# Performance work log

Measured on AMD Instinct MI355X. Metric: run time of the kernel, lower is better.

Reference implementation:

```python
import jax, jax.numpy as jnp
import numpy as np

IN_FEATURES = 4096
OUT_FEATURES = 1024
BATCH = 16384
WERR = 1.0
BERR = 1.0


def setup_inputs() -> dict:
    key = jax.random.key(0)
    kx, kw = jax.random.split(key)
    X = jax.random.normal(kx, (BATCH, IN_FEATURES), dtype=jnp.float32)
    # glorot_uniform init for W, zeros for bias (as in Keras layer)
    limit = np.sqrt(6.0 / (IN_FEATURES + OUT_FEATURES)).astype(np.float32)
    W = jax.random.uniform(kw, (IN_FEATURES, OUT_FEATURES), dtype=jnp.float32,
                           minval=-limit, maxval=limit)
    bias = jnp.zeros((1, OUT_FEATURES), dtype=jnp.float32)
    return {"X": X, "W": W, "bias": bias}


def reference(X, W, bias):
    # Binarize weights/bias with sign(), scaled by Werr/Berr, then dense matmul.
    Wb = jnp.sign(W) * WERR          # [in, out], values in {-1, 0, +1}
    bb = jnp.sign(bias) * BERR       # [1, out]
    Z = jnp.matmul(X, Wb) + bb       # [batch, out]
    return Z
```

## Files before the change

kernel.cpp:

```cpp
#include <hip/hip_runtime.h>

#define M_DIM 16384
#define N_DIM 1024
#define K_DIM 4096

#define BM 256
#define BN 256
#define BK 64
#define NT (K_DIM / BK)

typedef __attribute__((ext_vector_type(4))) float f32x4;
typedef __attribute__((ext_vector_type(8))) short bf16x8;
typedef __attribute__((ext_vector_type(8))) unsigned short u16x8;

static __device__ __forceinline__ short f2bf(float f) {
  union { __bf16 h; short s; } u;
  u.h = (__bf16)f;
  return u.s;
}

static __device__ __forceinline__ void load_lds16(const void* g, void* l) {
  __builtin_amdgcn_global_load_lds(
      (const __attribute__((address_space(1))) void*)g,
      (__attribute__((address_space(3))) void*)l, 16, 0, 0);
}

__global__ __launch_bounds__(256) void wsign_transpose(
    const float* __restrict__ W, unsigned short* __restrict__ WbT) {
  __shared__ unsigned short tile[64][72];
  const int t  = (int)threadIdx.x;
  const int k0 = (int)(blockIdx.x >> 4) * 64;
  const int n0 = (int)(blockIdx.x & 15) * 64;
#pragma unroll
  for (int p = 0; p < 4; ++p) {
    const int r = p * 16 + (t >> 4);
    const int c = (t & 15) * 4;
    const float* src = W + (size_t)(k0 + r) * N_DIM + n0 + c;
#pragma unroll
    for (int j = 0; j < 4; ++j) {
      const float w = src[j];
      tile[r][c + j] = (w > 0.f) ? (unsigned short)0x3F80u
                                 : ((w < 0.f) ? (unsigned short)0xBF80u
                                              : (unsigned short)0u);
    }
  }
  __syncthreads();
  const int n  = t >> 2;
  const int kg = (t & 3) * 16;
  u16x8 o0, o1;
#pragma unroll
  for (int j = 0; j < 8; ++j) o0[j] = tile[kg + j][n];
#pragma unroll
  for (int j = 0; j < 8; ++j) o1[j] = tile[kg + 8 + j][n];
  unsigned short* dst = WbT + (size_t)(n0 + n) * K_DIM + k0 + kg;
  *(u16x8*)dst       = o0;
  *(u16x8*)(dst + 8) = o1;
}

__global__ __launch_bounds__(512, 2) void gemm_bin(
    const float* __restrict__ X, const unsigned short* __restrict__ WbT,
    const float* __restrict__ bias, float* __restrict__ Z) {
  __shared__ __align__(16) unsigned short As[2][BM * BK];
  __shared__ __align__(16) unsigned short Bs[2][BN * BK];

  const int t   = (int)threadIdx.x;
  const int l   = t & 63;
  const int wid = t >> 6;
  const int wm  = wid >> 2;
  const int wn  = wid & 3;

  const int bid = (int)blockIdx.x;
  const int swz = (bid & 7) * 32 + (bid >> 3);
  const int m0  = (swz >> 2) * BM;
  const int n0  = (swz & 3) * BN;

  const int abase = (wm * 128 + (l & 15)) * BK;
  const int bbase = (wn * 64 + (l & 15)) * BK;
  const int axk0  = (((l >> 4) + 0) ^ (l & 7)) << 3;
  const int axk1  = (((l >> 4) + 4) ^ (l & 7)) << 3;

  const float* a_src[4];
  int a_dst[4];
#pragma unroll
  for (int i = 0; i < 4; ++i) {
    const int d = i * 512 + t;
    const int row = d >> 3, g = d & 7;
    a_src[i] = X + (size_t)(m0 + row) * K_DIM + g * 8;
    a_dst[i] = row * BK + ((g ^ (row & 7)) << 3);
  }
  const unsigned short* b_src[4];
  int b_dst[4];
#pragma unroll
  for (int i = 0; i < 4; ++i) {
    const int c = i * 512 + t;
    const int n = c >> 3, gp = c & 7;
    b_src[i] = WbT + (size_t)(n0 + n) * K_DIM + (gp ^ (n & 7)) * 8;
    b_dst[i] = c * 8;
  }

  f32x4 acc[8][4] = {};
  f32x4 areg[4][2];

#define STAGE_A_LOAD(KT)                                                  \
  {                                                                       \
    _Pragma("unroll") for (int i = 0; i < 4; ++i) {                       \
      areg[i][0] = *(const f32x4*)(a_src[i] + (KT));                      \
      areg[i][1] = *(const f32x4*)(a_src[i] + (KT) + 4);                  \
    }                                                                     \
  }
#define STAGE_A_WRITE(BUF)                                                \
  {                                                                       \
    _Pragma("unroll") for (int i = 0; i < 4; ++i) {                       \
      u16x8 v;                                                            \
      _Pragma("unroll") for (int j = 0; j < 4; ++j) {                     \
        v[j]     = (unsigned short)f2bf(areg[i][0][j]);                   \
        v[4 + j] = (unsigned short)f2bf(areg[i][1][j]);                   \
      }                                                                   \
      *(u16x8*)(&As[BUF][a_dst[i]]) = v;                                  \
    }                                                                     \
  }
#define STAGE_B(KT, BUF)                                                  \
  {                                                                       \
    _Pragma("unroll") for (int i = 0; i < 4; ++i)                         \
      load_lds16(b_src[i] + (KT), &Bs[BUF][b_dst[i]]);                    \
  }
#define COMPUTE(CUR)                                                      \
  {                                                                       \
    const unsigned short* Ab = As[CUR];                                   \
    const unsigned short* Bb = Bs[CUR];                                   \
    _Pragma("unroll") for (int kk = 0; kk < 2; ++kk) {                    \
      const int axk = kk ? axk1 : axk0;                                   \
      bf16x8 bf[4];                                                       \
      _Pragma("unroll") for (int ni = 0; ni < 4; ++ni)                    \
        bf[ni] = *(const bf16x8*)(Bb + bbase + ni * 1024 + axk);          \
      _Pragma("unroll") for (int mi = 0; mi < 8; ++mi) {                  \
        const bf16x8 af = *(const bf16x8*)(Ab + abase + mi * 1024 + axk); \
        _Pragma("unroll") for (int ni = 0; ni < 4; ++ni)                  \
          acc[mi][ni] = __builtin_amdgcn_mfma_f32_16x16x32_bf16(          \
              af, bf[ni], acc[mi][ni], 0, 0, 0);                          \
      }                                                                   \
    }                                                                     \
  }

  STAGE_A_LOAD(0);
  STAGE_B(0, 0);
  STAGE_A_WRITE(0);
  __syncthreads();

  int cur = 0;
  for (int tt = 0; tt < NT - 1; ++tt) {
    const int ktn = (tt + 1) * BK;
    STAGE_A_LOAD(ktn);
    STAGE_B(ktn, cur ^ 1);
    COMPUTE(cur);
    STAGE_A_WRITE(cur ^ 1);
    __syncthreads();
    cur ^= 1;
  }
  COMPUTE(cur);

#pragma unroll
  for (int ni = 0; ni < 4; ++ni) {
    const int col = n0 + wn * 64 + ni * 16 + (l & 15);
    const float b  = bias[col];
    const float bs = (b > 0.f) ? 1.f : ((b < 0.f) ? -1.f : 0.f);
#pragma unroll
    for (int mi = 0; mi < 8; ++mi) {
      const int row = m0 + wm * 128 + mi * 16 + ((l >> 4) << 2);
#pragma unroll
      for (int j = 0; j < 4; ++j)
        Z[(size_t)(row + j) * N_DIM + col] = acc[mi][ni][j] + bs;
    }
  }
#undef STAGE_A_LOAD
#undef STAGE_A_WRITE
#undef STAGE_B
#undef COMPUTE
}

__global__ __launch_bounds__(256) void naive_fb(
    const float* __restrict__ X, const float* __restrict__ W,
    const float* __restrict__ bias, float* __restrict__ Z) {
  const size_t id = (size_t)blockIdx.x * 256 + threadIdx.x;
  const int m = (int)(id >> 10), n = (int)(id & 1023);
  float acc = 0.f;
  for (int k = 0; k < K_DIM; ++k) {
    const float w = W[(size_t)k * N_DIM + n];
    const float s = (w > 0.f) ? 1.f : ((w < 0.f) ? -1.f : 0.f);
    acc += X[(size_t)m * K_DIM + k] * s;
  }
  const float b = bias[n];
  Z[id] = acc + ((b > 0.f) ? 1.f : ((b < 0.f) ? -1.f : 0.f));
}

extern "C" void kernel_launch(void* const* d_in, const int* in_sizes, int n_in,
                              void* d_out, int out_size, void* d_ws, size_t ws_size,
                              hipStream_t stream) {
  const float* X    = (const float*)d_in[0];
  const float* W    = (const float*)d_in[1];
  const float* bias = (const float*)d_in[2];
  float* Z = (float*)d_out;

  const size_t need = (size_t)N_DIM * K_DIM * sizeof(unsigned short);
  if (ws_size >= need) {
    unsigned short* WbT = (unsigned short*)d_ws;
    wsign_transpose<<<dim3((K_DIM / 64) * (N_DIM / 64)), dim3(256), 0, stream>>>(W, WbT);
    gemm_bin<<<dim3((M_DIM / BM) * (N_DIM / BN)), dim3(512), 0, stream>>>(X, WbT, bias, Z);
  } else {
    naive_fb<<<dim3((size_t)M_DIM * N_DIM / 256), dim3(256), 0, stream>>>(X, W, bias, Z);
  }
}
```

Before: 192.0 us.

## Restructure GEMM main loop into a quadrant-interleaved pipeline with explicit waitcnts

The GEMM main loop is rewritten as a hand-scheduled pipeline. Each K tile is split into four MFMA quadrants, and the LDS fragment reads, global loads of A and B for two tiles ahead, and A bf16 writes are interleaved between them. Explicit s_waitcnt, sched_barrier, s_barrier and setprio calls pin the instruction order so memory latency is hidden behind MFMA work. This adds many extra barriers per tile and relies on the prefetch-depth and LDS buffer-reuse ordering being correct.

```diff
diff --git a/kernel.cpp b/kernel.cpp
--- a/kernel.cpp
+++ b/kernel.cpp
@@ -100,64 +100,136 @@
 
   f32x4 acc[8][4] = {};
   f32x4 areg[4][2];
-
-#define STAGE_A_LOAD(KT)                                                  \
-  {                                                                       \
-    _Pragma("unroll") for (int i = 0; i < 4; ++i) {                       \
-      areg[i][0] = *(const f32x4*)(a_src[i] + (KT));                      \
-      areg[i][1] = *(const f32x4*)(a_src[i] + (KT) + 4);                  \
-    }                                                                     \
-  }
-#define STAGE_A_WRITE(BUF)                                                \
-  {                                                                       \
-    _Pragma("unroll") for (int i = 0; i < 4; ++i) {                       \
-      u16x8 v;                                                            \
-      _Pragma("unroll") for (int j = 0; j < 4; ++j) {                     \
-        v[j]     = (unsigned short)f2bf(areg[i][0][j]);                   \
-        v[4 + j] = (unsigned short)f2bf(areg[i][1][j]);                   \
-      }                                                                   \
-      *(u16x8*)(&As[BUF][a_dst[i]]) = v;                                  \
-    }                                                                     \
-  }
-#define STAGE_B(KT, BUF)                                                  \
-  {                                                                       \
-    _Pragma("unroll") for (int i = 0; i < 4; ++i)                         \
-      load_lds16(b_src[i] + (KT), &Bs[BUF][b_dst[i]]);                    \
-  }
-#define COMPUTE(CUR)                                                      \
-  {                                                                       \
-    const unsigned short* Ab = As[CUR];                                   \
-    const unsigned short* Bb = Bs[CUR];                                   \
-    _Pragma("unroll") for (int kk = 0; kk < 2; ++kk) {                    \
-      const int axk = kk ? axk1 : axk0;                                   \
-      bf16x8 bf[4];                                                       \
-      _Pragma("unroll") for (int ni = 0; ni < 4; ++ni)                    \
-        bf[ni] = *(const bf16x8*)(Bb + bbase + ni * 1024 + axk);          \
-      _Pragma("unroll") for (int mi = 0; mi < 8; ++mi) {                  \
-        const bf16x8 af = *(const bf16x8*)(Ab + abase + mi * 1024 + axk); \
-        _Pragma("unroll") for (int ni = 0; ni < 4; ++ni)                  \
-          acc[mi][ni] = __builtin_amdgcn_mfma_f32_16x16x32_bf16(          \
-              af, bf[ni], acc[mi][ni], 0, 0, 0);                          \
-      }                                                                   \
-    }                                                                     \
-  }
-
-  STAGE_A_LOAD(0);
-  STAGE_B(0, 0);
-  STAGE_A_WRITE(0);
-  __syncthreads();
-
-  int cur = 0;
-  for (int tt = 0; tt < NT - 1; ++tt) {
-    const int ktn = (tt + 1) * BK;
-    STAGE_A_LOAD(ktn);
-    STAGE_B(ktn, cur ^ 1);
-    COMPUTE(cur);
-    STAGE_A_WRITE(cur ^ 1);
-    __syncthreads();
-    cur ^= 1;
-  }
-  COMPUTE(cur);
+  bf16x8 aF[2][4], bN0[2][2], bN1[2][2];
+
+#define SB0 __builtin_amdgcn_sched_barrier(0)
+#define BAR do { SB0; __builtin_amdgcn_s_barrier(); SB0; } while (0)
+#define WVM(N) do { asm volatile("s_waitcnt vmcnt(" #N ")" ::: "memory"); SB0; } while (0)
+#define WLG do { asm volatile("s_waitcnt lgkmcnt(0)" ::: "memory"); SB0; } while (0)
+#define PRIO1 __builtin_amdgcn_s_setprio(1)
+#define PRIO0 __builtin_amdgcn_s_setprio(0)
+
+#define ISSUE_A(KT)                                                        \
+  do { SB0;                                                                \
+    _Pragma("unroll") for (int i = 0; i < 4; ++i) {                        \
+      areg[i][0] = *(const f32x4*)(a_src[i] + (KT));                       \
+      areg[i][1] = *(const f32x4*)(a_src[i] + (KT) + 4);                   \
+    } SB0;                                                                 \
+  } while (0)
+#define WRITE_A(BUF)                                                       \
+  do {                                                                     \
+    _Pragma("unroll") for (int i = 0; i < 4; ++i) {                        \
+      u16x8 v;                                                             \
+      _Pragma("unroll") for (int j = 0; j < 4; ++j) {                      \
+        v[j]     = (unsigned short)f2bf(areg[i][0][j]);                    \
+        v[4 + j] = (unsigned short)f2bf(areg[i][1][j]);                    \
+      }                                                                    \
+      *(u16x8*)(&As[BUF][a_dst[i]]) = v;                                   \
+    }                                                                      \
+  } while (0)
+#define ISSUE_B(KT, BUF)                                                   \
+  do { SB0;                                                                \
+    _Pragma("unroll") for (int i = 0; i < 4; ++i)                          \
+      load_lds16(b_src[i] + (KT), &Bs[BUF][b_dst[i]]);                     \
+    SB0;                                                                   \
+  } while (0)
+#define READ_A(MH, AB)                                                     \
+  do {                                                                     \
+    _Pragma("unroll") for (int mi = 0; mi < 4; ++mi) {                     \
+      aF[0][mi] = *(const bf16x8*)((AB) + abase + ((MH)*4 + mi) * 1024 + axk0); \
+      aF[1][mi] = *(const bf16x8*)((AB) + abase + ((MH)*4 + mi) * 1024 + axk1); \
+    }                                                                      \
+  } while (0)
+#define READ_B(NH, DST, BB)                                                \
+  do {                                                                     \
+    _Pragma("unroll") for (int ni = 0; ni < 2; ++ni) {                     \
+      DST[0][ni] = *(const bf16x8*)((BB) + bbase + ((NH)*2 + ni) * 1024 + axk0); \
+      DST[1][ni] = *(const bf16x8*)((BB) + bbase + ((NH)*2 + ni) * 1024 + axk1); \
+    }                                                                      \
+  } while (0)
+#define MFMA_Q(MH, NH, BF)                                                 \
+  do {                                                                     \
+    _Pragma("unroll") for (int kk = 0; kk < 2; ++kk)                       \
+      _Pragma("unroll") for (int mi = 0; mi < 4; ++mi)                     \
+        _Pragma("unroll") for (int ni = 0; ni < 2; ++ni)                   \
+          acc[(MH)*4 + mi][(NH)*2 + ni] =                                  \
+              __builtin_amdgcn_mfma_f32_16x16x32_bf16(                     \
+                  aF[kk][mi], BF[kk][ni], acc[(MH)*4 + mi][(NH)*2 + ni],   \
+                  0, 0, 0);                                                \
+  } while (0)
+
+  ISSUE_A(0);
+  ISSUE_B(0, 0);
+  WVM(4);
+  WRITE_A(0);
+  ISSUE_A(BK);
+  ISSUE_B(BK, 1);
+  WVM(12);
+  WLG;
+  BAR;
+
+  for (int tt = 0; tt <= NT - 3; ++tt) {
+    const int buf = tt & 1;
+    const unsigned short* Ab = As[buf];
+    const unsigned short* Bb = Bs[buf];
+    WVM(4);
+    WRITE_A(buf ^ 1);
+    READ_A(0, Ab);
+    READ_B(0, bN0, Bb);
+    BAR; WLG;
+    PRIO1; MFMA_Q(0, 0, bN0); PRIO0;
+    BAR;
+    ISSUE_A((tt + 2) * BK);
+    READ_B(1, bN1, Bb);
+    BAR; WLG;
+    PRIO1; MFMA_Q(0, 1, bN1); PRIO0;
+    BAR;
+    ISSUE_B((tt + 2) * BK, buf);
+    READ_A(1, Ab);
+    BAR; WLG;
+    PRIO1; MFMA_Q(1, 1, bN1); PRIO0;
+    BAR;
+    PRIO1; MFMA_Q(1, 0, bN0); PRIO0;
+    WVM(12);
+    BAR;
+  }
+
+  {
+    const int buf = (NT - 2) & 1;
+    const unsigned short* Ab = As[buf];
+    const unsigned short* Bb = Bs[buf];
+    WVM(4);
+    WRITE_A(buf ^ 1);
+    READ_A(0, Ab);
+    READ_B(0, bN0, Bb);
+    BAR; WLG;
+    PRIO1; MFMA_Q(0, 0, bN0); PRIO0;
+    BAR;
+    READ_B(1, bN1, Bb);
+    BAR; WLG;
+    PRIO1; MFMA_Q(0, 1, bN1); PRIO0;
+    BAR;
+    READ_A(1, Ab);
+    BAR; WLG;
+    PRIO1; MFMA_Q(1, 1, bN1); PRIO0;
+    BAR;
+    PRIO1; MFMA_Q(1, 0, bN0); PRIO0;
+    WVM(0);
+    BAR;
+  }
+  {
+    const int buf = (NT - 1) & 1;
+    const unsigned short* Ab = As[buf];
+    const unsigned short* Bb = Bs[buf];
+    READ_A(0, Ab);
+    READ_B(0, bN0, Bb);
+    READ_B(1, bN1, Bb);
+    MFMA_Q(0, 0, bN0);
+    MFMA_Q(0, 1, bN1);
+    READ_A(1, Ab);
+    MFMA_Q(1, 1, bN1);
+    MFMA_Q(1, 0, bN0);
+  }
 
 #pragma unroll
   for (int ni = 0; ni < 4; ++ni) {
@@ -172,10 +244,18 @@
         Z[(size_t)(row + j) * N_DIM + col] = acc[mi][ni][j] + bs;
     }
   }
-#undef STAGE_A_LOAD
-#undef STAGE_A_WRITE
-#undef STAGE_B
-#undef COMPUTE
+#undef SB0
+#undef BAR
+#undef WVM
+#undef WLG
+#undef PRIO1
+#undef PRIO0
+#undef ISSUE_A
+#undef WRITE_A
+#undef ISSUE_B
+#undef READ_A
+#undef READ_B
+#undef MFMA_Q
 }
 
 __global__ __launch_bounds__(256) void naive_fb(
```

Result: no change. 188.4 us (-1.9%).

## Pre-convert X to bf16 and pipeline GEMM with DMA A-tiles and register B

Applied to the files above, without the earlier changes.

Adds a separate pass that converts X from fp32 to bf16 into workspace. A new GEMM kernel can then stream A tiles straight into LDS with global_load_lds, and it loads B fragments directly from global into registers instead of staging them in LDS. The main loop is hand-scheduled with sched barriers, explicit waitcnts and setprio to overlap loads with MFMA. The cost is an extra 256MB read plus 128MB write pass over X, and the path needs a larger workspace; when that workspace is missing it falls back to the old fused kernel.

```diff
diff --git a/kernel.cpp b/kernel.cpp
--- a/kernel.cpp
+++ b/kernel.cpp
@@ -23,6 +23,23 @@
   __builtin_amdgcn_global_load_lds(
       (const __attribute__((address_space(1))) void*)g,
       (__attribute__((address_space(3))) void*)l, 16, 0, 0);
+}
+
+__global__ __launch_bounds__(256) void xcvt(
+    const float* __restrict__ X, unsigned short* __restrict__ Xb) {
+  const size_t n8 = (size_t)M_DIM * K_DIM / 8;
+  const size_t stride = (size_t)gridDim.x * 256;
+  for (size_t i = (size_t)blockIdx.x * 256 + threadIdx.x; i < n8; i += stride) {
+    const f32x4 v0 = *(const f32x4*)(X + i * 8);
+    const f32x4 v1 = *(const f32x4*)(X + i * 8 + 4);
+    u16x8 o;
+#pragma unroll
+    for (int j = 0; j < 4; ++j) {
+      o[j]     = (unsigned short)f2bf(v0[j]);
+      o[4 + j] = (unsigned short)f2bf(v1[j]);
+    }
+    *(u16x8*)(Xb + i * 8) = o;
+  }
 }
 
 __global__ __launch_bounds__(256) void wsign_transpose(
@@ -57,7 +74,144 @@
   *(u16x8*)(dst + 8) = o1;
 }
 
-__global__ __launch_bounds__(512, 2) void gemm_bin(
+__global__ __launch_bounds__(512, 2) void gemm_dma(
+    const unsigned short* __restrict__ Xb, const unsigned short* __restrict__ WbT,
+    const float* __restrict__ bias, float* __restrict__ Z) {
+  __shared__ __align__(16) unsigned short As[2][BM * BK];
+
+  const int t   = (int)threadIdx.x;
+  const int l   = t & 63;
+  const int wid = t >> 6;
+  const int wm  = wid >> 2;
+  const int wn  = wid & 3;
+
+  const int bid = (int)blockIdx.x;
+  const int swz = (bid & 7) * 32 + (bid >> 3);
+  const int m0  = (swz >> 2) * BM;
+  const int n0  = (swz & 3) * BN;
+
+  const int abase = (wm * 128 + (l & 15)) * BK;
+  const int axk0  = (((l >> 4) + 0) ^ (l & 7)) << 3;
+  const int axk1  = (((l >> 4) + 4) ^ (l & 7)) << 3;
+
+  const unsigned short* a_src[4];
+  int a_dst[4];
+#pragma unroll
+  for (int i = 0; i < 4; ++i) {
+    const int c = i * 512 + t;
+    const int r = c >> 3, g = c & 7;
+    a_src[i] = Xb + (size_t)(m0 + r) * K_DIM + (g ^ (r & 7)) * 8;
+    a_dst[i] = c * 8;
+  }
+  const unsigned short* bp[4];
+#pragma unroll
+  for (int ni = 0; ni < 4; ++ni)
+    bp[ni] = WbT + (size_t)(n0 + wn * 64 + ni * 16 + (l & 15)) * K_DIM +
+             (l >> 4) * 8;
+
+  f32x4 acc[8][4] = {};
+  bf16x8 aF0[2][4], aF1[2][4];
+  bf16x8 PB0[2][2], PB1[2][2];
+
+#define SB0 __builtin_amdgcn_sched_barrier(0)
+#define BAR do { SB0; __builtin_amdgcn_s_barrier(); SB0; } while (0)
+#define WVM(N) do { asm volatile("s_waitcnt vmcnt(" #N ")" ::: "memory"); SB0; } while (0)
+#define WLG0 do { asm volatile("s_waitcnt lgkmcnt(0)" ::: "memory"); SB0; } while (0)
+
+#define DMA_A(KT, BUF)                                                     \
+  do { SB0;                                                                \
+    _Pragma("unroll") for (int i = 0; i < 4; ++i)                          \
+      load_lds16(a_src[i] + (KT), &As[BUF][a_dst[i]]);                     \
+    SB0;                                                                   \
+  } while (0)
+#define LD_PB(SET, NIB, KT)                                                \
+  do { SB0;                                                                \
+    _Pragma("unroll") for (int kk = 0; kk < 2; ++kk)                       \
+      _Pragma("unroll") for (int nj = 0; nj < 2; ++nj)                     \
+        SET[kk][nj] = *(const bf16x8*)(bp[(NIB) + nj] + (KT) + kk * 32);   \
+    SB0;                                                                   \
+  } while (0)
+#define RD_A(DST, MH, AB)                                                  \
+  do { SB0;                                                                \
+    _Pragma("unroll") for (int mi = 0; mi < 4; ++mi) {                     \
+      DST[0][mi] = *(const bf16x8*)((AB) + abase + ((MH)*4 + mi) * 1024 + axk0); \
+      DST[1][mi] = *(const bf16x8*)((AB) + abase + ((MH)*4 + mi) * 1024 + axk1); \
+    } SB0;                                                                 \
+  } while (0)
+#define Q(MH, NH, AFR, BSET)                                               \
+  do { __builtin_amdgcn_s_setprio(1);                                      \
+    _Pragma("unroll") for (int kk = 0; kk < 2; ++kk)                       \
+      _Pragma("unroll") for (int mi = 0; mi < 4; ++mi)                     \
+        _Pragma("unroll") for (int nj = 0; nj < 2; ++nj)                   \
+          acc[(MH)*4 + mi][(NH)*2 + nj] =                                  \
+              __builtin_amdgcn_mfma_f32_16x16x32_bf16(                     \
+                  AFR[kk][mi], BSET[kk][nj], acc[(MH)*4 + mi][(NH)*2 + nj],\
+                  0, 0, 0);                                                \
+    __builtin_amdgcn_s_setprio(0);                                         \
+  } while (0)
+
+  DMA_A(0, 0);
+  LD_PB(PB1, 2, 0);
+  LD_PB(PB0, 0, 0);
+  WVM(8);
+  BAR;
+
+  for (int tt = 0; tt < NT - 1; ++tt) {
+    const unsigned short* Ab = As[tt & 1];
+    const int ktn = (tt + 1) * BK;
+    DMA_A(ktn, (tt + 1) & 1);
+    RD_A(aF0, 0, Ab);
+    WVM(4);
+    WLG0;
+    Q(0, 0, aF0, PB0);
+    RD_A(aF1, 1, Ab);
+    Q(0, 1, aF0, PB1);
+    WLG0;
+    Q(1, 1, aF1, PB1);
+    LD_PB(PB1, 2, ktn);
+    Q(1, 0, aF1, PB0);
+    LD_PB(PB0, 0, ktn);
+    WVM(8);
+    BAR;
+  }
+
+  {
+    const unsigned short* Ab = As[(NT - 1) & 1];
+    RD_A(aF0, 0, Ab);
+    WVM(0);
+    WLG0;
+    Q(0, 0, aF0, PB0);
+    RD_A(aF1, 1, Ab);
+    Q(0, 1, aF0, PB1);
+    WLG0;
+    Q(1, 1, aF1, PB1);
+    Q(1, 0, aF1, PB0);
+  }
+
+#pragma unroll
+  for (int ni = 0; ni < 4; ++ni) {
+    const int col = n0 + wn * 64 + ni * 16 + (l & 15);
+    const float b  = bias[col];
+    const float bs = (b > 0.f) ? 1.f : ((b < 0.f) ? -1.f : 0.f);
+#pragma unroll
+    for (int mi = 0; mi < 8; ++mi) {
+      const int row = m0 + wm * 128 + mi * 16 + ((l >> 4) << 2);
+#pragma unroll
+      for (int j = 0; j < 4; ++j)
+        Z[(size_t)(row + j) * N_DIM + col] = acc[mi][ni][j] + bs;
+    }
+  }
+#undef SB0
+#undef BAR
+#undef WVM
+#undef WLG0
+#undef DMA_A
+#undef LD_PB
+#undef RD_A
+#undef Q
+}
+
+__global__ __launch_bounds__(512, 2) void gemm_fused(
     const float* __restrict__ X, const unsigned short* __restrict__ WbT,
     const float* __restrict__ bias, float* __restrict__ Z) {
   __shared__ __align__(16) unsigned short As[2][BM * BK];
@@ -201,11 +355,18 @@
   const float* bias = (const float*)d_in[2];
   float* Z = (float*)d_out;
 
-  const size_t need = (size_t)N_DIM * K_DIM * sizeof(unsigned short);
-  if (ws_size >= need) {
+  const size_t needW = (size_t)N_DIM * K_DIM * sizeof(unsigned short);
+  const size_t needX = (size_t)M_DIM * K_DIM * sizeof(unsigned short);
+  if (ws_size >= needW + needX) {
+    unsigned short* WbT = (unsigned short*)d_ws;
+    unsigned short* Xb  = (unsigned short*)((char*)d_ws + needW);
+    xcvt<<<dim3(2048), dim3(256), 0, stream>>>(X, Xb);
+    wsign_transpose<<<dim3((K_DIM / 64) * (N_DIM / 64)), dim3(256), 0, stream>>>(W, WbT);
+    gemm_dma<<<dim3((M_DIM / BM) * (N_DIM / BN)), dim3(512), 0, stream>>>(Xb, WbT, bias, Z);
+  } else if (ws_size >= needW) {
     unsigned short* WbT = (unsigned short*)d_ws;
     wsign_transpose<<<dim3((K_DIM / 64) * (N_DIM / 64)), dim3(256), 0, stream>>>(W, WbT);
-    gemm_bin<<<dim3((M_DIM / BM) * (N_DIM / BN)), dim3(512), 0, stream>>>(X, WbT, bias, Z);
+    gemm_fused<<<dim3((M_DIM / BM) * (N_DIM / BN)), dim3(512), 0, stream>>>(X, WbT, bias, Z);
   } else {
     naive_fb<<<dim3((size_t)M_DIM * N_DIM / 256), dim3(256), 0, stream>>>(X, W, bias, Z);
   }
```

After: 255.4 us. 33.1% more time.

## Restructure GEMM main loop into phased schedule interleaving loads, LDS writes and MFMA quadrants

Applied to the files above, without the earlier changes.

The GEMM inner loop is split into four compute quadrants (M-half by N-half). Global loads of X, DMA of B tiles, bf16 conversion writes to LDS and LDS fragment reads are interleaved between the quadrants, with explicit barriers, waitcnt and sched_barrier fences, plus s_setprio raised around the MFMA bursts. The aim is to hide memory latency behind matrix-core work and cut the register pressure of staging the whole A tile at once. The cost is many more block-wide barriers per K-step and a schedule that leans on hand-placed wait counts, which could stall waves if they are wrong.

```diff
diff --git a/kernel.cpp b/kernel.cpp
--- a/kernel.cpp
+++ b/kernel.cpp
@@ -57,7 +57,7 @@
   *(u16x8*)(dst + 8) = o1;
 }
 
-__global__ __launch_bounds__(512, 2) void gemm_bin(
+__global__ __launch_bounds__(512, 2) void gemm_8ph(
     const float* __restrict__ X, const unsigned short* __restrict__ WbT,
     const float* __restrict__ bias, float* __restrict__ Z) {
   __shared__ __align__(16) unsigned short As[2][BM * BK];
@@ -79,15 +79,12 @@
   const int axk0  = (((l >> 4) + 0) ^ (l & 7)) << 3;
   const int axk1  = (((l >> 4) + 4) ^ (l & 7)) << 3;
 
-  const float* a_src[4];
-  int a_dst[4];
-#pragma unroll
-  for (int i = 0; i < 4; ++i) {
-    const int d = i * 512 + t;
-    const int row = d >> 3, g = d & 7;
-    a_src[i] = X + (size_t)(m0 + row) * K_DIM + g * 8;
-    a_dst[i] = row * BK + ((g ^ (row & 7)) << 3);
-  }
+  const float* sA[4];
+#pragma unroll
+  for (int i = 0; i < 4; ++i)
+    sA[i] = X + (size_t)(m0 + i * 64 + (t >> 3)) * K_DIM + (t & 7) * 8;
+  const int adst = (t >> 3) * BK + (((t & 7) ^ ((t >> 3) & 7)) << 3);
+
   const unsigned short* b_src[4];
   int b_dst[4];
 #pragma unroll
@@ -99,65 +96,117 @@
   }
 
   f32x4 acc[8][4] = {};
-  f32x4 areg[4][2];
-
-#define STAGE_A_LOAD(KT)                                                  \
-  {                                                                       \
-    _Pragma("unroll") for (int i = 0; i < 4; ++i) {                       \
-      areg[i][0] = *(const f32x4*)(a_src[i] + (KT));                      \
-      areg[i][1] = *(const f32x4*)(a_src[i] + (KT) + 4);                  \
-    }                                                                     \
-  }
-#define STAGE_A_WRITE(BUF)                                                \
-  {                                                                       \
-    _Pragma("unroll") for (int i = 0; i < 4; ++i) {                       \
-      u16x8 v;                                                            \
-      _Pragma("unroll") for (int j = 0; j < 4; ++j) {                     \
-        v[j]     = (unsigned short)f2bf(areg[i][0][j]);                   \
-        v[4 + j] = (unsigned short)f2bf(areg[i][1][j]);                   \
-      }                                                                   \
-      *(u16x8*)(&As[BUF][a_dst[i]]) = v;                                  \
-    }                                                                     \
-  }
-#define STAGE_B(KT, BUF)                                                  \
-  {                                                                       \
-    _Pragma("unroll") for (int i = 0; i < 4; ++i)                         \
-      load_lds16(b_src[i] + (KT), &Bs[BUF][b_dst[i]]);                    \
-  }
-#define COMPUTE(CUR)                                                      \
-  {                                                                       \
-    const unsigned short* Ab = As[CUR];                                   \
-    const unsigned short* Bb = Bs[CUR];                                   \
-    _Pragma("unroll") for (int kk = 0; kk < 2; ++kk) {                    \
-      const int axk = kk ? axk1 : axk0;                                   \
-      bf16x8 bf[4];                                                       \
-      _Pragma("unroll") for (int ni = 0; ni < 4; ++ni)                    \
-        bf[ni] = *(const bf16x8*)(Bb + bbase + ni * 1024 + axk);          \
-      _Pragma("unroll") for (int mi = 0; mi < 8; ++mi) {                  \
-        const bf16x8 af = *(const bf16x8*)(Ab + abase + mi * 1024 + axk); \
-        _Pragma("unroll") for (int ni = 0; ni < 4; ++ni)                  \
-          acc[mi][ni] = __builtin_amdgcn_mfma_f32_16x16x32_bf16(          \
-              af, bf[ni], acc[mi][ni], 0, 0, 0);                          \
-      }                                                                   \
-    }                                                                     \
-  }
-
-  STAGE_A_LOAD(0);
-  STAGE_B(0, 0);
-  STAGE_A_WRITE(0);
-  __syncthreads();
-
-  int cur = 0;
+  f32x4 ar[2][2];
+  bf16x8 aF[2][4];
+  bf16x8 bF0[2][2], bF1[2][2];
+
+#define SB0 __builtin_amdgcn_sched_barrier(0)
+#define BAR do { SB0; __builtin_amdgcn_s_barrier(); SB0; } while (0)
+#define WVM(N) do { asm volatile("s_waitcnt vmcnt(" #N ")" ::: "memory"); SB0; } while (0)
+#define WLG0 do { asm volatile("s_waitcnt lgkmcnt(0)" ::: "memory"); SB0; } while (0)
+
+#define LD_AH(H, KT)                                                       \
+  do { SB0;                                                                \
+    ar[0][0] = *(const f32x4*)(sA[2 * (H)] + (KT));                        \
+    ar[0][1] = *(const f32x4*)(sA[2 * (H)] + (KT) + 4);                    \
+    ar[1][0] = *(const f32x4*)(sA[2 * (H) + 1] + (KT));                    \
+    ar[1][1] = *(const f32x4*)(sA[2 * (H) + 1] + (KT) + 4); SB0;           \
+  } while (0)
+#define WR_AH(H, BUF)                                                      \
+  do {                                                                     \
+    _Pragma("unroll") for (int j = 0; j < 2; ++j) {                        \
+      u16x8 v;                                                             \
+      _Pragma("unroll") for (int q = 0; q < 4; ++q) {                      \
+        v[q]     = (unsigned short)f2bf(ar[j][0][q]);                      \
+        v[4 + q] = (unsigned short)f2bf(ar[j][1][q]);                      \
+      }                                                                    \
+      *(u16x8*)(&As[BUF][adst + (2 * (H) + j) * 4096]) = v;                \
+    }                                                                      \
+  } while (0)
+#define DMA_B2(KT, BUF, I0)                                                \
+  do { SB0;                                                                \
+    _Pragma("unroll") for (int i = (I0); i < (I0) + 2; ++i)                \
+      load_lds16(b_src[i] + (KT), &Bs[BUF][b_dst[i]]);                     \
+    SB0;                                                                   \
+  } while (0)
+#define RD_A(MH, AB)                                                       \
+  do { SB0;                                                                \
+    _Pragma("unroll") for (int mi = 0; mi < 4; ++mi) {                     \
+      aF[0][mi] = *(const bf16x8*)((AB) + abase + ((MH)*4 + mi) * 1024 + axk0); \
+      aF[1][mi] = *(const bf16x8*)((AB) + abase + ((MH)*4 + mi) * 1024 + axk1); \
+    } SB0;                                                                 \
+  } while (0)
+#define RD_B(DST, NH, BB)                                                  \
+  do { SB0;                                                                \
+    _Pragma("unroll") for (int nj = 0; nj < 2; ++nj) {                     \
+      DST[0][nj] = *(const bf16x8*)((BB) + bbase + ((NH)*2 + nj) * 1024 + axk0); \
+      DST[1][nj] = *(const bf16x8*)((BB) + bbase + ((NH)*2 + nj) * 1024 + axk1); \
+    } SB0;                                                                 \
+  } while (0)
+#define Q(MH, NH, BF)                                                      \
+  do { __builtin_amdgcn_s_setprio(1);                                      \
+    _Pragma("unroll") for (int kk = 0; kk < 2; ++kk)                       \
+      _Pragma("unroll") for (int mi = 0; mi < 4; ++mi)                     \
+        _Pragma("unroll") for (int nj = 0; nj < 2; ++nj)                   \
+          acc[(MH)*4 + mi][(NH)*2 + nj] =                                  \
+              __builtin_amdgcn_mfma_f32_16x16x32_bf16(                     \
+                  aF[kk][mi], BF[kk][nj], acc[(MH)*4 + mi][(NH)*2 + nj],   \
+                  0, 0, 0);                                                \
+    __builtin_amdgcn_s_setprio(0);                                         \
+  } while (0)
+
+  LD_AH(0, 0); WVM(0); WR_AH(0, 0);
+  LD_AH(1, 0); WVM(0); WR_AH(1, 0);
+  DMA_B2(0, 0, 0); DMA_B2(0, 0, 2);
+  WVM(0); WLG0;
+  BAR;
+
   for (int tt = 0; tt < NT - 1; ++tt) {
+    const int cur = tt & 1, nxt = cur ^ 1;
+    const unsigned short* Ab = As[cur];
+    const unsigned short* Bb = Bs[cur];
     const int ktn = (tt + 1) * BK;
-    STAGE_A_LOAD(ktn);
-    STAGE_B(ktn, cur ^ 1);
-    COMPUTE(cur);
-    STAGE_A_WRITE(cur ^ 1);
-    __syncthreads();
-    cur ^= 1;
-  }
-  COMPUTE(cur);
+    RD_A(0, Ab);
+    RD_B(bF0, 0, Bb);
+    LD_AH(0, ktn);
+    BAR; WLG0;
+    Q(0, 0, bF0);
+    BAR;
+    RD_B(bF1, 1, Bb);
+    DMA_B2(ktn, nxt, 0);
+    WVM(2);
+    WR_AH(0, nxt);
+    BAR; WLG0;
+    Q(0, 1, bF1);
+    BAR;
+    RD_A(1, Ab);
+    LD_AH(1, ktn);
+    DMA_B2(ktn, nxt, 2);
+    BAR; WLG0;
+    Q(1, 1, bF1);
+    BAR;
+    WVM(0);
+    WR_AH(1, nxt);
+    Q(1, 0, bF0);
+    WLG0;
+    BAR;
+  }
+
+  {
+    const unsigned short* Ab = As[(NT - 1) & 1];
+    const unsigned short* Bb = Bs[(NT - 1) & 1];
+    RD_A(0, Ab);
+    RD_B(bF0, 0, Bb);
+    WLG0;
+    Q(0, 0, bF0);
+    RD_B(bF1, 1, Bb);
+    WLG0;
+    Q(0, 1, bF1);
+    RD_A(1, Ab);
+    WLG0;
+    Q(1, 1, bF1);
+    Q(1, 0, bF0);
+  }
 
 #pragma unroll
   for (int ni = 0; ni < 4; ++ni) {
@@ -172,10 +221,16 @@
         Z[(size_t)(row + j) * N_DIM + col] = acc[mi][ni][j] + bs;
     }
   }
-#undef STAGE_A_LOAD
-#undef STAGE_A_WRITE
-#undef STAGE_B
-#undef COMPUTE
+#undef SB0
+#undef BAR
+#undef WVM
+#undef WLG0
+#undef LD_AH
+#undef WR_AH
+#undef DMA_B2
+#undef RD_A
+#undef RD_B
+#undef Q
 }
 
 __global__ __launch_bounds__(256) void naive_fb(
@@ -201,11 +256,11 @@
   const float* bias = (const float*)d_in[2];
   float* Z = (float*)d_out;
 
-  const size_t need = (size_t)N_DIM * K_DIM * sizeof(unsigned short);
-  if (ws_size >= need) {
+  const size_t needW = (size_t)N_DIM * K_DIM * sizeof(unsigned short);
+  if (ws_size >= needW) {
     unsigned short* WbT = (unsigned short*)d_ws;
     wsign_transpose<<<dim3((K_DIM / 64) * (N_DIM / 64)), dim3(256), 0, stream>>>(W, WbT);
-    gemm_bin<<<dim3((M_DIM / BM) * (N_DIM / BN)), dim3(512), 0, stream>>>(X, WbT, bias, Z);
+    gemm_8ph<<<dim3((M_DIM / BM) * (N_DIM / BN)), dim3(512), 0, stream>>>(X, WbT, bias, Z);
   } else {
     naive_fb<<<dim3((size_t)M_DIM * N_DIM / 256), dim3(256), 0, stream>>>(X, W, bias, Z);
   }
```

After: 202.5 us. +5.5%, slower.
